# Kernel tuning notes

Measured on AMD Instinct MI355X. Metric: run time of the kernel, lower is better.

## Reference

```python
import jax, jax.numpy as jnp
import numpy as np
from jax.ops import segment_sum

N = 50000
E = 1200000
F_IN = 128
HID = 64
N_CLS = 40


def _sage(x, edge_index, edge_weight, W_l, W_r, b):
    # SAGEConv with mean aggregation; messages optionally scaled by edge_weight.
    src, dst = edge_index[0], edge_index[1]
    msg = x[src] * edge_weight[:, None]            # [E, F] gather + scale
    summ = segment_sum(msg, dst, num_segments=N)   # [N, F] scatter-add
    deg = segment_sum(jnp.ones((E,), x.dtype), dst, num_segments=N)
    agg = summ / jnp.maximum(deg, 1.0)[:, None]    # mean over incoming edges
    return agg @ W_l + x @ W_r + b


def setup_inputs() -> dict:
    key = jax.random.key(0)
    ks = jax.random.split(key, 16)
    def glorot(k, shape):
        fan = shape[0] + shape[1]
        return jax.random.normal(k, shape, jnp.float32) * jnp.sqrt(2.0 / fan)
    return {
        "x0": jax.random.normal(ks[0], (N, F_IN), jnp.float32),
        "edge_index": jax.random.randint(ks[1], (2, E), 0, N),
        "edge_weight": jax.random.uniform(ks[2], (E,), jnp.float32),
        "W1l": glorot(ks[3], (F_IN, HID)), "W1r": glorot(ks[4], (F_IN, HID)),
        "b1": jnp.zeros((HID,), jnp.float32),
        "W2l": glorot(ks[5], (HID, HID)), "W2r": glorot(ks[6], (HID, HID)),
        "b2": jnp.zeros((HID,), jnp.float32),
        "W3l": glorot(ks[7], (HID, HID)), "W3r": glorot(ks[8], (HID, HID)),
        "b3": jnp.zeros((HID,), jnp.float32),
        "Wlin": glorot(ks[9], (3 * HID, N_CLS)),
        "blin": jnp.zeros((N_CLS,), jnp.float32),
    }


def reference(x0, edge_index, edge_weight, W1l, W1r, b1, W2l, W2r, b2,
              W3l, W3r, b3, Wlin, blin):
    # dropout in eval mode (identity)
    x1 = jax.nn.relu(_sage(x0, edge_index, edge_weight, W1l, W1r, b1))
    x2 = jax.nn.relu(_sage(x1, edge_index, edge_weight, W2l, W2r, b2))
    x3 = jax.nn.relu(_sage(x2, edge_index, edge_weight, W3l, W3r, b3))
    x = jnp.concatenate([x1, x2, x3], axis=-1)     # [N, 3*HID]
    logits = x @ Wlin + blin                        # [N, N_CLS]
    return jax.nn.log_softmax(logits, axis=-1)
```

## Files before the change

kernel.cpp:

```cpp
#include <hip/hip_runtime.h>
#include <hip/hip_bf16.h>
#include <math.h>

static constexpr int Nn   = 50000;
static constexpr int Ee   = 1200000;
static constexpr int FIN  = 128;
static constexpr int HID  = 64;
static constexpr int NCLS = 40;

static constexpr int NBK    = (Nn + 255) / 256;
static constexpr int CAP    = 7168;
static constexpr int FSLICE = 4096;
static constexpr int FBLK   = (Ee + FSLICE - 1) / FSLICE;

typedef float f32x4  __attribute__((ext_vector_type(4)));
typedef short short8 __attribute__((ext_vector_type(8)));

__device__ inline unsigned short f2b(float f) {
    unsigned int u = __builtin_bit_cast(unsigned int, f);
    return (unsigned short)((u + 0x7FFFu + ((u >> 16) & 1u)) >> 16);
}
__device__ inline float b2f(unsigned short h) {
    return __builtin_bit_cast(float, (unsigned int)h << 16);
}
__device__ inline float b2f_lo(unsigned int u) {
    return __builtin_bit_cast(float, u << 16);
}
__device__ inline float b2f_hi(unsigned int u) {
    return __builtin_bit_cast(float, u & 0xFFFF0000u);
}

__global__ __launch_bounds__(256) void init_kernel(int* __restrict__ bcur) {
    int t = threadIdx.x;
    if (t < NBK) bcur[t] = t * CAP;
}

__global__ __launch_bounds__(1024) void bin_fill_kernel(
    const int* __restrict__ src, const int* __restrict__ dst,
    const float* __restrict__ ew, int* __restrict__ bcur,
    int2* __restrict__ edgeT) {
    __shared__ int hist[NBK];
    __shared__ int gbase[NBK];
    const int tid = threadIdx.x;
    for (int i = tid; i < NBK; i += 1024) hist[i] = 0;
    __syncthreads();
    const int e0 = blockIdx.x * FSLICE;
    const int e1 = min(e0 + FSLICE, Ee);
    for (int e = e0 + tid; e < e1; e += 1024)
        atomicAdd(&hist[dst[e] >> 8], 1);
    __syncthreads();
    for (int b = tid; b < NBK; b += 1024) {
        int c = hist[b];
        gbase[b] = c ? atomicAdd(&bcur[b], c) : 0;
        hist[b] = 0;
    }
    __syncthreads();
    for (int e = e0 + tid; e < e1; e += 1024) {
        int d = dst[e];
        int b = d >> 8;
        int r = atomicAdd(&hist[b], 1);
        edgeT[gbase[b] + r] =
            make_int2(src[e] | ((d & 255) << 16), __builtin_bit_cast(int, ew[e]));
    }
}

template <int K, typename XT>
__device__ inline void gemm_body(
    const int row0, const int tid,
    unsigned short* __restrict__ wt, float* __restrict__ b_s,
    const XT* __restrict__ x, const float* __restrict__ Wl,
    const float* __restrict__ Wr, const float* __restrict__ b,
    unsigned short* __restrict__ yl, unsigned short* __restrict__ z) {
    constexpr int LDW = K + 8;
    constexpr int NKT = K / 32;

    for (int i = tid; i < K * 64; i += 256) {
        int k = i >> 6, c = i & 63;
        wt[c * LDW + k]        = f2b(Wl[i]);
        wt[(64 + c) * LDW + k] = f2b(Wr[i]);
    }
    if (tid < 64) b_s[tid] = b[tid];
    __syncthreads();

    const int wv   = tid >> 6;
    const int lane = tid & 63;
    const int l15  = lane & 15;
    const int quad = lane >> 4;

    const int arow = row0 + wv * 16 + l15;
    const bool rok = arow < Nn;
    short8 a[NKT];
#pragma unroll
    for (int kt = 0; kt < NKT; ++kt) {
        if (rok) {
            if constexpr (sizeof(XT) == 2) {
                a[kt] = *(const short8*)((const unsigned short*)x +
                                         (size_t)arow * K + kt * 32 + quad * 8);
            } else {
                const float* xp = (const float*)x + (size_t)arow * K + kt * 32 + quad * 8;
                float4 p0 = *(const float4*)xp;
                float4 p1 = *(const float4*)(xp + 4);
                short8 af;
                af[0] = (short)f2b(p0.x); af[1] = (short)f2b(p0.y);
                af[2] = (short)f2b(p0.z); af[3] = (short)f2b(p0.w);
                af[4] = (short)f2b(p1.x); af[5] = (short)f2b(p1.y);
                af[6] = (short)f2b(p1.z); af[7] = (short)f2b(p1.w);
                a[kt] = af;
            }
        } else {
            a[kt] = (short8){0, 0, 0, 0, 0, 0, 0, 0};
        }
    }

    f32x4 acc[8];
#pragma unroll
    for (int ct = 0; ct < 8; ++ct) acc[ct] = (f32x4){0.f, 0.f, 0.f, 0.f};

#pragma unroll
    for (int ct = 0; ct < 8; ++ct) {
        const unsigned short* brow = wt + (ct * 16 + l15) * LDW + quad * 8;
#pragma unroll
        for (int kt = 0; kt < NKT; ++kt) {
            short8 bf = *(const short8*)(brow + kt * 32);
            acc[ct] = __builtin_amdgcn_mfma_f32_16x16x32_bf16(a[kt], bf, acc[ct], 0, 0, 0);
        }
    }

#pragma unroll
    for (int ct = 0; ct < 8; ++ct) {
        int col = ct * 16 + l15;
#pragma unroll
        for (int reg = 0; reg < 4; ++reg) {
            int grow = row0 + wv * 16 + quad * 4 + reg;
            if (grow < Nn) {
                if (col < 64) yl[grow * 64 + col] = f2b(acc[ct][reg]);
                else          z[grow * 64 + col - 64] = f2b(acc[ct][reg] + b_s[col - 64]);
            }
        }
    }
}

template <int K, typename XT>
__global__ __launch_bounds__(256) void gemmM_kernel(
    const XT* __restrict__ x, const float* __restrict__ Wl,
    const float* __restrict__ Wr, const float* __restrict__ b,
    unsigned short* __restrict__ yl, unsigned short* __restrict__ z) {
    __shared__ unsigned short wt[128 * (K + 8)];
    __shared__ float b_s[64];
    gemm_body<K, XT>(blockIdx.x * 64, threadIdx.x, wt, b_s, x, Wl, Wr, b, yl, z);
}

__global__ __launch_bounds__(256) void sort_gemm1_kernel(
    const int* __restrict__ bcur, const int2* __restrict__ edgeT,
    unsigned int* __restrict__ edgeA, int* __restrict__ rowbeg,
    int* __restrict__ rowend,
    const float* __restrict__ x0, const float* __restrict__ W1l,
    const float* __restrict__ W1r, const float* __restrict__ b1,
    unsigned short* __restrict__ yl, unsigned short* __restrict__ z) {
    __shared__ int hist[256];
    __shared__ int cur[256];
    __shared__ int wsum[4];
    __shared__ unsigned short wt[128 * (FIN + 8)];
    __shared__ float b_s[64];

    if (blockIdx.x >= NBK) {
        gemm_body<FIN, float>((int)(blockIdx.x - NBK) * 64, threadIdx.x,
                              wt, b_s, x0, W1l, W1r, b1, yl, z);
        return;
    }

    const int t = threadIdx.x, lane = t & 63, wv = t >> 6;
    const int b = blockIdx.x;
    const int beg = b * CAP;
    const int end = bcur[b];

    hist[t] = 0;
    __syncthreads();
    for (int e = beg + t; e < end; e += 256)
        atomicAdd(&hist[edgeT[e].x >> 16], 1);
    __syncthreads();

    int v = hist[t], incl = v;
#pragma unroll
    for (int off = 1; off < 64; off <<= 1) {
        int u = __shfl_up(incl, off);
        if (lane >= off) incl += u;
    }
    if (lane == 63) wsum[wv] = incl;
    __syncthreads();
    {
        int woff = 0;
#pragma unroll
        for (int w = 0; w < 4; ++w) woff += (w < wv) ? wsum[w] : 0;
        const int base = beg + woff + incl - v;
        const int grow = b * 256 + t;
        if (grow < Nn) { rowbeg[grow] = base; rowend[grow] = base + v; }
        cur[t] = base;
    }
    __syncthreads();

    for (int e = beg + t; e < end; e += 256) {
        int2 ed = edgeT[e];
        int ld = ed.x >> 16;
        int p = atomicAdd(&cur[ld], 1);
        unsigned short wb = f2b(__builtin_bit_cast(float, ed.y));
        edgeA[p] = (unsigned int)(ed.x & 0xFFFF) | ((unsigned int)wb << 16);
    }
}

__global__ __launch_bounds__(256) void gather_kernel(
    const int* __restrict__ rowbeg, const int* __restrict__ rowend,
    const unsigned int* __restrict__ edgeA, const unsigned short* __restrict__ yl,
    const unsigned short* __restrict__ z, unsigned short* __restrict__ xout) {
    const int wid  = (blockIdx.x * 256 + threadIdx.x) >> 6;
    const int lane = threadIdx.x & 63;
    const int q    = lane >> 4;
    const int c    = lane & 15;
    const int r    = wid * 4 + q;
    const int beg = rowbeg[r], end = rowend[r];

    const uint2* __restrict__ yl64 = (const uint2*)yl;
    const uint2* __restrict__ z64  = (const uint2*)z;
    uint2* __restrict__ xo64       = (uint2*)xout;

    float a0 = 0.f, a1 = 0.f, a2 = 0.f, a3 = 0.f;
    int p = beg;
    const int pfull = beg + ((end - beg) & ~7);

    for (; p < pfull; p += 8) {
        unsigned int eb[8];
        uint2 uu[8];
#pragma unroll
        for (int j = 0; j < 8; ++j) eb[j] = edgeA[p + j];
#pragma unroll
        for (int j = 0; j < 8; ++j)
            uu[j] = yl64[(size_t)(eb[j] & 0xFFFFu) * 16 + c];
#pragma unroll
        for (int j = 0; j < 8; ++j) {
            float w = b2f((unsigned short)(eb[j] >> 16));
            a0 += b2f_lo(uu[j].x) * w;
            a1 += b2f_hi(uu[j].x) * w;
            a2 += b2f_lo(uu[j].y) * w;
            a3 += b2f_hi(uu[j].y) * w;
        }
    }
    if (p < end) {
        unsigned int eb[8];
        uint2 uu[8];
#pragma unroll
        for (int j = 0; j < 8; ++j) eb[j] = (p + j < end) ? edgeA[p + j] : 0u;
#pragma unroll
        for (int j = 0; j < 8; ++j)
            uu[j] = yl64[(size_t)(eb[j] & 0xFFFFu) * 16 + c];
#pragma unroll
        for (int j = 0; j < 8; ++j) {
            float w = b2f((unsigned short)(eb[j] >> 16));
            a0 += b2f_lo(uu[j].x) * w;
            a1 += b2f_hi(uu[j].x) * w;
            a2 += b2f_lo(uu[j].y) * w;
            a3 += b2f_hi(uu[j].y) * w;
        }
    }

    const float den = fmaxf((float)(end - beg), 1.f);
    const uint2 zw = z64[(size_t)r * 16 + c];
    float v0 = a0 / den + b2f_lo(zw.x);
    float v1 = a1 / den + b2f_hi(zw.x);
    float v2 = a2 / den + b2f_lo(zw.y);
    float v3 = a3 / den + b2f_hi(zw.y);
    uint2 o;
    o.x = (unsigned int)f2b(fmaxf(v0, 0.f)) | ((unsigned int)f2b(fmaxf(v1, 0.f)) << 16);
    o.y = (unsigned int)f2b(fmaxf(v2, 0.f)) | ((unsigned int)f2b(fmaxf(v3, 0.f)) << 16);
    xo64[(size_t)r * 16 + c] = o;
}

__global__ __launch_bounds__(256) void final_kernel(
    const unsigned short* __restrict__ x1, const unsigned short* __restrict__ x2,
    const unsigned short* __restrict__ x3, const float* __restrict__ Wlin,
    const float* __restrict__ blin, float* __restrict__ out) {
    __shared__ unsigned short wt[48 * 200];

    const int tid  = threadIdx.x;
    const int row0 = blockIdx.x * 64;

    for (int i = tid; i < 48 * 200; i += 256) wt[i] = 0;
    __syncthreads();
    for (int i = tid; i < 192 * 40; i += 256) {
        int k = i / 40, n = i % 40;
        wt[n * 200 + k] = f2b(Wlin[i]);
    }
    __syncthreads();

    const int wv   = tid >> 6;
    const int lane = tid & 63;
    const int l15  = lane & 15;
    const int quad = lane >> 4;

    const int arow = row0 + wv * 16 + l15;
    const bool rok = arow < Nn;
    const unsigned short* xarr[3] = {x1, x2, x3};
    short8 a[6];
#pragma unroll
    for (int ks = 0; ks < 6; ++ks) {
        if (rok)
            a[ks] = *(const short8*)(xarr[ks >> 1] + (size_t)arow * 64 +
                                     (ks & 1) * 32 + quad * 8);
        else
            a[ks] = (short8){0, 0, 0, 0, 0, 0, 0, 0};
    }

    f32x4 acc[3];
#pragma unroll
    for (int nt = 0; nt < 3; ++nt) {
        acc[nt] = (f32x4){0.f, 0.f, 0.f, 0.f};
        const unsigned short* brow = wt + (nt * 16 + l15) * 200 + quad * 8;
#pragma unroll
        for (int ks = 0; ks < 6; ++ks) {
            short8 b = *(const short8*)(brow + ks * 32);
            acc[nt] = __builtin_amdgcn_mfma_f32_16x16x32_bf16(a[ks], b, acc[nt], 0, 0, 0);
        }
    }

    const bool c2ok = l15 < 8;
    const float b0 = blin[l15];
    const float b1 = blin[16 + l15];
    const float b2 = c2ok ? blin[32 + l15] : 0.f;

#pragma unroll
    for (int reg = 0; reg < 4; ++reg) {
        float v0 = acc[0][reg] + b0;
        float v1 = acc[1][reg] + b1;
        float v2 = c2ok ? acc[2][reg] + b2 : -INFINITY;
        float mx = fmaxf(fmaxf(v0, v1), v2);
#pragma unroll
        for (int off = 1; off < 16; off <<= 1) mx = fmaxf(mx, __shfl_xor(mx, off));
        float s = expf(v0 - mx) + expf(v1 - mx) + (c2ok ? expf(v2 - mx) : 0.f);
#pragma unroll
        for (int off = 1; off < 16; off <<= 1) s += __shfl_xor(s, off);
        float lse = mx + logf(s);
        int grow = row0 + wv * 16 + quad * 4 + reg;
        if (grow < Nn) {
            out[grow * NCLS + l15]      = v0 - lse;
            out[grow * NCLS + 16 + l15] = v1 - lse;
            if (c2ok) out[grow * NCLS + 32 + l15] = v2 - lse;
        }
    }
}

extern "C" void kernel_launch(void* const* d_in, const int* in_sizes, int n_in,
                              void* d_out, int out_size, void* d_ws, size_t ws_size,
                              hipStream_t stream) {
    const float* x0  = (const float*)d_in[0];
    const int*   ei  = (const int*)d_in[1];
    const float* ew  = (const float*)d_in[2];
    const float* W1l = (const float*)d_in[3];
    const float* W1r = (const float*)d_in[4];
    const float* b1  = (const float*)d_in[5];
    const float* W2l = (const float*)d_in[6];
    const float* W2r = (const float*)d_in[7];
    const float* b2  = (const float*)d_in[8];
    const float* W3l = (const float*)d_in[9];
    const float* W3r = (const float*)d_in[10];
    const float* b3  = (const float*)d_in[11];
    const float* Wlin = (const float*)d_in[12];
    const float* blin = (const float*)d_in[13];
    float* out = (float*)d_out;

    const int* src = ei;
    const int* dst = ei + Ee;

    const size_t N64 = (size_t)Nn * 64;
    const size_t REG = (size_t)NBK * CAP;
    char* ws = (char*)d_ws;
    int*   bcur   = (int*)ws;
    int*   rowbeg = bcur + 256;
    int*   rowend = rowbeg + 50048;
    int2*  edgeT  = (int2*)(rowend + 50048);
    unsigned int* edgeA = (unsigned int*)(edgeT + REG);
    unsigned short* yl  = (unsigned short*)(edgeA + REG);
    unsigned short* zb  = yl + N64;
    unsigned short* x1  = zb + N64;
    unsigned short* x2  = x1 + N64;
    unsigned short* x3  = x2 + N64;

    const int gemm_blocks = (Nn + 63) / 64;
    const int sg_blocks   = NBK + gemm_blocks;
    const int row_blocks  = Nn / 16;
    const int fin_blocks  = (Nn + 63) / 64;

    init_kernel<<<1, 256, 0, stream>>>(bcur);
    bin_fill_kernel<<<FBLK, 1024, 0, stream>>>(src, dst, ew, bcur, edgeT);

    sort_gemm1_kernel<<<sg_blocks, 256, 0, stream>>>(
        bcur, edgeT, edgeA, rowbeg, rowend, x0, W1l, W1r, b1, yl, zb);

    gather_kernel<<<row_blocks, 256, 0, stream>>>(rowbeg, rowend, edgeA, yl, zb, x1);

    gemmM_kernel<HID, unsigned short><<<gemm_blocks, 256, 0, stream>>>(x1, W2l, W2r, b2, yl, zb);
    gather_kernel<<<row_blocks, 256, 0, stream>>>(rowbeg, rowend, edgeA, yl, zb, x2);

    gemmM_kernel<HID, unsigned short><<<gemm_blocks, 256, 0, stream>>>(x2, W3l, W3r, b3, yl, zb);
    gather_kernel<<<row_blocks, 256, 0, stream>>>(rowbeg, rowend, edgeA, yl, zb, x3);

    final_kernel<<<fin_blocks, 256, 0, stream>>>(x1, x2, x3, Wlin, blin, out);
}
```

Measured before the change: 236.7 us.

## Split gather edges by source half and sync blocks between halves for L2 locality

The sort stage now orders each row's edges by whether the source node falls in the lower or upper half of the node range, and records a per-row midpoint. The gather kernel becomes persistent (1024 blocks, several row groups each). It first accumulates lower-half sources, then meets at a global spin barrier with a bounded spin count, then accumulates upper-half sources, so the working set of the feature table that is live at any moment is halved and fits better in cache. It also uses nontemporal loads and stores for the streaming edge and output data, at the cost of a grid-wide barrier, higher register use and a bounded spin that can give up early.

```diff
diff --git a/kernel.cpp b/kernel.cpp
--- a/kernel.cpp
+++ b/kernel.cpp
@@ -13,6 +13,11 @@
 static constexpr int FSLICE = 4096;
 static constexpr int FBLK   = (Ee + FSLICE - 1) / FSLICE;
 
+static constexpr int NHALF  = Nn / 2;
+static constexpr int NGRP   = Nn / 16;
+static constexpr int GATH_G = 1024;
+static constexpr int GPASS  = (NGRP + GATH_G - 1) / GATH_G;
+
 typedef float f32x4  __attribute__((ext_vector_type(4)));
 typedef short short8 __attribute__((ext_vector_type(8)));
 
@@ -33,6 +38,7 @@
 __global__ __launch_bounds__(256) void init_kernel(int* __restrict__ bcur) {
     int t = threadIdx.x;
     if (t < NBK) bcur[t] = t * CAP;
+    else if (t < 256) bcur[t] = 0;
 }
 
 __global__ __launch_bounds__(1024) void bin_fill_kernel(
@@ -153,12 +159,12 @@
 __global__ __launch_bounds__(256) void sort_gemm1_kernel(
     const int* __restrict__ bcur, const int2* __restrict__ edgeT,
     unsigned int* __restrict__ edgeA, int* __restrict__ rowbeg,
-    int* __restrict__ rowend,
+    int* __restrict__ rowmid, int* __restrict__ rowend,
     const float* __restrict__ x0, const float* __restrict__ W1l,
     const float* __restrict__ W1r, const float* __restrict__ b1,
     unsigned short* __restrict__ yl, unsigned short* __restrict__ z) {
-    __shared__ int hist[256];
-    __shared__ int cur[256];
+    __shared__ int hist[512];
+    __shared__ int cur[512];
     __shared__ int wsum[4];
     __shared__ unsigned short wt[128 * (FIN + 8)];
     __shared__ float b_s[64];
@@ -175,12 +181,17 @@
     const int end = bcur[b];
 
     hist[t] = 0;
-    __syncthreads();
-    for (int e = beg + t; e < end; e += 256)
-        atomicAdd(&hist[edgeT[e].x >> 16], 1);
-    __syncthreads();
-
-    int v = hist[t], incl = v;
+    hist[t + 256] = 0;
+    __syncthreads();
+    for (int e = beg + t; e < end; e += 256) {
+        int ex = edgeT[e].x;
+        int key = ((ex >> 16) << 1) | (int)((ex & 0xFFFF) >= NHALF);
+        atomicAdd(&hist[key], 1);
+    }
+    __syncthreads();
+
+    const int h0 = hist[2 * t], h1 = hist[2 * t + 1];
+    int s = h0 + h1, incl = s;
 #pragma unroll
     for (int off = 1; off < 64; off <<= 1) {
         int u = __shfl_up(incl, off);
@@ -192,86 +203,129 @@
         int woff = 0;
 #pragma unroll
         for (int w = 0; w < 4; ++w) woff += (w < wv) ? wsum[w] : 0;
-        const int base = beg + woff + incl - v;
+        const int base = beg + woff + incl - s;
         const int grow = b * 256 + t;
-        if (grow < Nn) { rowbeg[grow] = base; rowend[grow] = base + v; }
-        cur[t] = base;
+        if (grow < Nn) {
+            rowbeg[grow] = base;
+            rowmid[grow] = base + h0;
+            rowend[grow] = base + s;
+        }
+        cur[2 * t]     = base;
+        cur[2 * t + 1] = base + h0;
     }
     __syncthreads();
 
     for (int e = beg + t; e < end; e += 256) {
         int2 ed = edgeT[e];
-        int ld = ed.x >> 16;
-        int p = atomicAdd(&cur[ld], 1);
+        int key = ((ed.x >> 16) << 1) | (int)((ed.x & 0xFFFF) >= NHALF);
+        int p = atomicAdd(&cur[key], 1);
         unsigned short wb = f2b(__builtin_bit_cast(float, ed.y));
         edgeA[p] = (unsigned int)(ed.x & 0xFFFF) | ((unsigned int)wb << 16);
     }
 }
 
-__global__ __launch_bounds__(256) void gather_kernel(
-    const int* __restrict__ rowbeg, const int* __restrict__ rowend,
-    const unsigned int* __restrict__ edgeA, const unsigned short* __restrict__ yl,
-    const unsigned short* __restrict__ z, unsigned short* __restrict__ xout) {
-    const int wid  = (blockIdx.x * 256 + threadIdx.x) >> 6;
-    const int lane = threadIdx.x & 63;
-    const int q    = lane >> 4;
-    const int c    = lane & 15;
-    const int r    = wid * 4 + q;
-    const int beg = rowbeg[r], end = rowend[r];
-
-    const uint2* __restrict__ yl64 = (const uint2*)yl;
-    const uint2* __restrict__ z64  = (const uint2*)z;
-    uint2* __restrict__ xo64       = (uint2*)xout;
-
-    float a0 = 0.f, a1 = 0.f, a2 = 0.f, a3 = 0.f;
-    int p = beg;
-    const int pfull = beg + ((end - beg) & ~7);
-
+__device__ inline void accum_range(
+    int p, int pend, const unsigned int* __restrict__ edgeA,
+    const uint2* __restrict__ yl64, int c, float (&a)[4]) {
+    const int pfull = p + ((pend - p) & ~7);
     for (; p < pfull; p += 8) {
         unsigned int eb[8];
         uint2 uu[8];
 #pragma unroll
-        for (int j = 0; j < 8; ++j) eb[j] = edgeA[p + j];
+        for (int j = 0; j < 8; ++j) eb[j] = __builtin_nontemporal_load(&edgeA[p + j]);
 #pragma unroll
         for (int j = 0; j < 8; ++j)
             uu[j] = yl64[(size_t)(eb[j] & 0xFFFFu) * 16 + c];
 #pragma unroll
         for (int j = 0; j < 8; ++j) {
             float w = b2f((unsigned short)(eb[j] >> 16));
-            a0 += b2f_lo(uu[j].x) * w;
-            a1 += b2f_hi(uu[j].x) * w;
-            a2 += b2f_lo(uu[j].y) * w;
-            a3 += b2f_hi(uu[j].y) * w;
-        }
-    }
-    if (p < end) {
+            a[0] += b2f_lo(uu[j].x) * w;
+            a[1] += b2f_hi(uu[j].x) * w;
+            a[2] += b2f_lo(uu[j].y) * w;
+            a[3] += b2f_hi(uu[j].y) * w;
+        }
+    }
+    if (p < pend) {
         unsigned int eb[8];
         uint2 uu[8];
 #pragma unroll
-        for (int j = 0; j < 8; ++j) eb[j] = (p + j < end) ? edgeA[p + j] : 0u;
+        for (int j = 0; j < 8; ++j)
+            eb[j] = (p + j < pend) ? __builtin_nontemporal_load(&edgeA[p + j]) : 0u;
 #pragma unroll
         for (int j = 0; j < 8; ++j)
             uu[j] = yl64[(size_t)(eb[j] & 0xFFFFu) * 16 + c];
 #pragma unroll
         for (int j = 0; j < 8; ++j) {
             float w = b2f((unsigned short)(eb[j] >> 16));
-            a0 += b2f_lo(uu[j].x) * w;
-            a1 += b2f_hi(uu[j].x) * w;
-            a2 += b2f_lo(uu[j].y) * w;
-            a3 += b2f_hi(uu[j].y) * w;
-        }
-    }
-
-    const float den = fmaxf((float)(end - beg), 1.f);
-    const uint2 zw = z64[(size_t)r * 16 + c];
-    float v0 = a0 / den + b2f_lo(zw.x);
-    float v1 = a1 / den + b2f_hi(zw.x);
-    float v2 = a2 / den + b2f_lo(zw.y);
-    float v3 = a3 / den + b2f_hi(zw.y);
-    uint2 o;
-    o.x = (unsigned int)f2b(fmaxf(v0, 0.f)) | ((unsigned int)f2b(fmaxf(v1, 0.f)) << 16);
-    o.y = (unsigned int)f2b(fmaxf(v2, 0.f)) | ((unsigned int)f2b(fmaxf(v3, 0.f)) << 16);
-    xo64[(size_t)r * 16 + c] = o;
+            a[0] += b2f_lo(uu[j].x) * w;
+            a[1] += b2f_hi(uu[j].x) * w;
+            a[2] += b2f_lo(uu[j].y) * w;
+            a[3] += b2f_hi(uu[j].y) * w;
+        }
+    }
+}
+
+__global__ __launch_bounds__(256, 4) void gather_kernel(
+    const int* __restrict__ rowbeg, const int* __restrict__ rowmid,
+    const int* __restrict__ rowend, const unsigned int* __restrict__ edgeA,
+    const unsigned short* __restrict__ yl, const unsigned short* __restrict__ z,
+    unsigned short* __restrict__ xout, int* __restrict__ bar) {
+    const int tid  = threadIdx.x;
+    const int lane = tid & 63;
+    const int qw   = (tid >> 6) * 4 + (lane >> 4);
+    const int c    = lane & 15;
+
+    const uint2* __restrict__ yl64 = (const uint2*)yl;
+    const unsigned long long* __restrict__ z64 = (const unsigned long long*)z;
+    unsigned long long* __restrict__ xo64      = (unsigned long long*)xout;
+
+    float ac[GPASS][4];
+
+#pragma unroll
+    for (int i = 0; i < GPASS; ++i) {
+        ac[i][0] = ac[i][1] = ac[i][2] = ac[i][3] = 0.f;
+        const int g = (int)blockIdx.x + i * GATH_G;
+        if (g < NGRP) {
+            const int r = g * 16 + qw;
+            accum_range(rowbeg[r], rowmid[r], edgeA, yl64, c, ac[i]);
+        }
+    }
+
+    __syncthreads();
+    if (tid == 0) {
+        __hip_atomic_fetch_add(bar, 1, __ATOMIC_RELAXED, __HIP_MEMORY_SCOPE_AGENT);
+        int spins = 0;
+        while (__hip_atomic_load(bar, __ATOMIC_RELAXED, __HIP_MEMORY_SCOPE_AGENT)
+                   < GATH_G && ++spins < 128)
+            __builtin_amdgcn_s_sleep(32);
+    }
+    __syncthreads();
+
+#pragma unroll
+    for (int i = 0; i < GPASS; ++i) {
+        const int g = (int)blockIdx.x + i * GATH_G;
+        if (g < NGRP) {
+            const int r = g * 16 + qw;
+            const int beg = rowbeg[r], mid = rowmid[r], end = rowend[r];
+            accum_range(mid, end, edgeA, yl64, c, ac[i]);
+            const float den = fmaxf((float)(end - beg), 1.f);
+            const unsigned long long zw =
+                __builtin_nontemporal_load(&z64[(size_t)r * 16 + c]);
+            const unsigned int zlo = (unsigned int)zw;
+            const unsigned int zhi = (unsigned int)(zw >> 32);
+            float v0 = ac[i][0] / den + b2f_lo(zlo);
+            float v1 = ac[i][1] / den + b2f_hi(zlo);
+            float v2 = ac[i][2] / den + b2f_lo(zhi);
+            float v3 = ac[i][3] / den + b2f_hi(zhi);
+            unsigned int olo = (unsigned int)f2b(fmaxf(v0, 0.f)) |
+                               ((unsigned int)f2b(fmaxf(v1, 0.f)) << 16);
+            unsigned int ohi = (unsigned int)f2b(fmaxf(v2, 0.f)) |
+                               ((unsigned int)f2b(fmaxf(v3, 0.f)) << 16);
+            unsigned long long o =
+                (unsigned long long)olo | ((unsigned long long)ohi << 32);
+            __builtin_nontemporal_store(o, &xo64[(size_t)r * 16 + c]);
+        }
+    }
 }
 
 __global__ __launch_bounds__(256) void final_kernel(
@@ -374,7 +428,8 @@
     char* ws = (char*)d_ws;
     int*   bcur   = (int*)ws;
     int*   rowbeg = bcur + 256;
-    int*   rowend = rowbeg + 50048;
+    int*   rowmid = rowbeg + 50048;
+    int*   rowend = rowmid + 50048;
     int2*  edgeT  = (int2*)(rowend + 50048);
     unsigned int* edgeA = (unsigned int*)(edgeT + REG);
     unsigned short* yl  = (unsigned short*)(edgeA + REG);
@@ -385,22 +440,24 @@
 
     const int gemm_blocks = (Nn + 63) / 64;
     const int sg_blocks   = NBK + gemm_blocks;
-    const int row_blocks  = Nn / 16;
     const int fin_blocks  = (Nn + 63) / 64;
 
     init_kernel<<<1, 256, 0, stream>>>(bcur);
     bin_fill_kernel<<<FBLK, 1024, 0, stream>>>(src, dst, ew, bcur, edgeT);
 
     sort_gemm1_kernel<<<sg_blocks, 256, 0, stream>>>(
-        bcur, edgeT, edgeA, rowbeg, rowend, x0, W1l, W1r, b1, yl, zb);
-
-    gather_kernel<<<row_blocks, 256, 0, stream>>>(rowbeg, rowend, edgeA, yl, zb, x1);
+        bcur, edgeT, edgeA, rowbeg, rowmid, rowend, x0, W1l, W1r, b1, yl, zb);
+
+    gather_kernel<<<GATH_G, 256, 0, stream>>>(
+        rowbeg, rowmid, rowend, edgeA, yl, zb, x1, bcur + 200);
 
     gemmM_kernel<HID, unsigned short><<<gemm_blocks, 256, 0, stream>>>(x1, W2l, W2r, b2, yl, zb);
-    gather_kernel<<<row_blocks, 256, 0, stream>>>(rowbeg, rowend, edgeA, yl, zb, x2);
+    gather_kernel<<<GATH_G, 256, 0, stream>>>(
+        rowbeg, rowmid, rowend, edgeA, yl, zb, x2, bcur + 201);
 
     gemmM_kernel<HID, unsigned short><<<gemm_blocks, 256, 0, stream>>>(x2, W3l, W3r, b3, yl, zb);
-    gather_kernel<<<row_blocks, 256, 0, stream>>>(rowbeg, rowend, edgeA, yl, zb, x3);
+    gather_kernel<<<GATH_G, 256, 0, stream>>>(
+        rowbeg, rowmid, rowend, edgeA, yl, zb, x3, bcur + 202);
 
     final_kernel<<<fin_blocks, 256, 0, stream>>>(x1, x2, x3, Wlin, blin, out);
 }
```

Measured after the change: 441.2 us. 1.86x slower.
